# Performance work log

Measured on AMD Instinct MI355X. Metric: run time of the kernel, lower is better.

The kernel has to match this reference:

```python
import jax, jax.numpy as jnp
import numpy as np

B, S, H, NH = 4, 1024, 1024, 16
HD = H // NH
CAUSAL_HEADS = 4
META_HEADS = NH // 4
CAUSAL_W = 0.7                      # cognitive_state['reasoning']['causal_active'] > 0.5 -> branch on
META_W = ((0.9 - 0.8) / 0.2) * 0.3  # awareness_level = 0.9 > 0.8 -> meta branch on, blend = 0.15


def _mha(xq, xkv, Win, bi, Wout, bout, nh):
    """torch nn.MultiheadAttention (batch_first) with packed in_proj [H, 3H]."""
    b, sq, h = xq.shape
    sk = xkv.shape[1]
    hd = h // nh
    q = (xq @ Win[:, :h] + bi[:h]).reshape(b, sq, nh, hd).transpose(0, 2, 1, 3)
    k = (xkv @ Win[:, h:2 * h] + bi[h:2 * h]).reshape(b, sk, nh, hd).transpose(0, 2, 1, 3)
    v = (xkv @ Win[:, 2 * h:] + bi[2 * h:]).reshape(b, sk, nh, hd).transpose(0, 2, 1, 3)
    scores = jnp.einsum('bhqd,bhkd->bhqk', q, k) / jnp.sqrt(jnp.asarray(hd, q.dtype))
    probs = jax.nn.softmax(scores, axis=-1)
    ctx = jnp.einsum('bhqk,bhkd->bhqd', probs, v)
    return ctx.transpose(0, 2, 1, 3).reshape(b, sq, h) @ Wout + bout


def _forward(hidden_states, cons_vec, Wq, bq, Wk, bk, Wv, bv, cg_W, cg_b, am_W, am_b,
             ca_Win, ca_bin, ca_Wout, ca_bout, mc_Win, mc_bin, mc_Wout, mc_bout, Wo, bo):
    b, s, h = hidden_states.shape
    q = (hidden_states @ Wq + bq).reshape(b, s, NH, HD).transpose(0, 2, 1, 3)
    k = (hidden_states @ Wk + bk).reshape(b, s, NH, HD).transpose(0, 2, 1, 3)
    v = (hidden_states @ Wv + bv).reshape(b, s, NH, HD).transpose(0, 2, 1, 3)
    scores = jnp.einsum('bhqd,bhkd->bhqk', q, k) / jnp.sqrt(jnp.asarray(HD, q.dtype))
    # consciousness-gated score modulation: sigmoid(gate(x) + awareness(cons_vec)) per (query, head)
    mod = jax.nn.sigmoid(hidden_states @ cg_W + cg_b + (cons_vec @ am_W + am_b))  # [B,S,NH]
    scores = scores * mod.transpose(0, 2, 1)[..., None]  # [B,NH,S,1] broadcast over keys
    probs = jax.nn.softmax(scores, axis=-1)
    ctx = jnp.einsum('bhqk,bhkd->bhqd', probs, v).transpose(0, 2, 1, 3).reshape(b, s, h)
    # causal MHA branch (active: causal_active=0.7 > 0.5)
    causal_ctx = _mha(hidden_states, hidden_states, ca_Win, ca_bin, ca_Wout, ca_bout, CAUSAL_HEADS)
    ctx = ctx * (1.0 - CAUSAL_W) + causal_ctx * CAUSAL_W
    # metacognitive MHA branch (active: awareness=0.9 > 0.8)
    meta_ctx = _mha(ctx, ctx, mc_Win, mc_bin, mc_Wout, mc_bout, META_HEADS)
    ctx = ctx * (1.0 - META_W) + meta_ctx * META_W
    return ctx @ Wo + bo


def setup_inputs() -> dict:
    key = jax.random.key(0)
    ks = jax.random.split(key, 16)
    sc = 0.02
    d = {
        'hidden_states': jax.random.normal(ks[0], (B, S, H), jnp.float32),
        'cons_vec': jax.random.uniform(ks[1], (16,), jnp.float32),
        'Wq': jax.random.normal(ks[2], (H, H), jnp.float32) * sc, 'bq': jnp.zeros((H,), jnp.float32),
        'Wk': jax.random.normal(ks[3], (H, H), jnp.float32) * sc, 'bk': jnp.zeros((H,), jnp.float32),
        'Wv': jax.random.normal(ks[4], (H, H), jnp.float32) * sc, 'bv': jnp.zeros((H,), jnp.float32),
        'cg_W': jax.random.normal(ks[5], (H, NH), jnp.float32) * sc, 'cg_b': jnp.zeros((NH,), jnp.float32),
        'am_W': jax.random.normal(ks[6], (16, NH), jnp.float32) * sc, 'am_b': jnp.zeros((NH,), jnp.float32),
        'ca_Win': jax.random.normal(ks[7], (H, 3 * H), jnp.float32) * sc, 'ca_bin': jnp.zeros((3 * H,), jnp.float32),
        'ca_Wout': jax.random.normal(ks[8], (H, H), jnp.float32) * sc, 'ca_bout': jnp.zeros((H,), jnp.float32),
        'mc_Win': jax.random.normal(ks[9], (H, 3 * H), jnp.float32) * sc, 'mc_bin': jnp.zeros((3 * H,), jnp.float32),
        'mc_Wout': jax.random.normal(ks[10], (H, H), jnp.float32) * sc, 'mc_bout': jnp.zeros((H,), jnp.float32),
        'Wo': jax.random.normal(ks[11], (H, H), jnp.float32) * sc, 'bo': jnp.zeros((H,), jnp.float32),
    }
    return d


def reference(hidden_states, cons_vec, Wq, bq, Wk, bk, Wv, bv, cg_W, cg_b, am_W, am_b,
              ca_Win, ca_bin, ca_Wout, ca_bout, mc_Win, mc_bin, mc_Wout, mc_bout, Wo, bo):
    return _forward(hidden_states, cons_vec, Wq, bq, Wk, bk, Wv, bv, cg_W, cg_b, am_W, am_b,
                    ca_Win, ca_bin, ca_Wout, ca_bout, mc_Win, mc_bin, mc_Wout, mc_bout, Wo, bo)
```

## Files before the change

### kernel.cpp

```cpp
#include <hip/hip_runtime.h>
#include <stdint.h>

typedef unsigned short u16;
typedef __attribute__((ext_vector_type(8))) short short8;
typedef __attribute__((ext_vector_type(4))) float f32x4;
typedef __attribute__((ext_vector_type(16))) float f32x16;

#define MFMA16(a,b,c) __builtin_amdgcn_mfma_f32_16x16x32_bf16((a),(b),(c),0,0,0)
#define MFMA32(a,b,c) __builtin_amdgcn_mfma_f32_32x32x16_bf16((a),(b),(c),0,0,0)

__device__ __forceinline__ float fast_exp2(float x) {
  return __builtin_amdgcn_exp2f(x);
}

__device__ __forceinline__ u16 f2bf(float f) {
  union { float f; uint32_t u; } v; v.f = f;
  uint32_t r = v.u + 0x7FFFu + ((v.u >> 16) & 1u);
  return (u16)(r >> 16);
}
__device__ __forceinline__ float bf2f(uint32_t u) {
  union { uint32_t i; float f; } v; v.i = u << 16; return v.f;
}
__device__ __forceinline__ void async_copy16(void* lds, const void* g) {
  __builtin_amdgcn_global_load_lds(
      (const __attribute__((address_space(1))) uint32_t*)g,
      (__attribute__((address_space(3))) uint32_t*)lds, 16, 0, 0);
}

__device__ __forceinline__ void transpose8x8(uint32_t r[4], int lane8) {
  uint32_t a0, a1, a2, a3;
  a0 = __shfl_xor(r[0], 4); a1 = __shfl_xor(r[1], 4);
  a2 = __shfl_xor(r[2], 4); a3 = __shfl_xor(r[3], 4);
  if (lane8 & 4) { r[0] = a2; r[1] = a3; } else { r[2] = a0; r[3] = a1; }
  a0 = __shfl_xor(r[0], 2); a1 = __shfl_xor(r[1], 2);
  a2 = __shfl_xor(r[2], 2); a3 = __shfl_xor(r[3], 2);
  if (lane8 & 2) { r[0] = a1; r[2] = a3; } else { r[1] = a0; r[3] = a2; }
  a0 = __shfl_xor(r[0], 1); a1 = __shfl_xor(r[1], 1);
  a2 = __shfl_xor(r[2], 1); a3 = __shfl_xor(r[3], 1);
  uint32_t sel = (lane8 & 1) ? 0x03020706u : 0x05040100u;
  r[0] = __builtin_amdgcn_perm(a0, r[0], sel);
  r[1] = __builtin_amdgcn_perm(a1, r[1], sel);
  r[2] = __builtin_amdgcn_perm(a2, r[2], sel);
  r[3] = __builtin_amdgcn_perm(a3, r[3], sel);
}

__global__ __launch_bounds__(256) void castmod_kernel(
    const float* __restrict__ X, u16* __restrict__ Xbf,
    const float* __restrict__ cgW, const float* __restrict__ cgb,
    const float* __restrict__ cons, const float* __restrict__ amW,
    const float* __restrict__ amb, float* __restrict__ modp) {
  __shared__ float xs[1024];
  __shared__ float part[16][16];
  __shared__ float am[16];
  int row = blockIdx.x, t = threadIdx.x;
  {
    float4 v = ((const float4*)(X + (size_t)row * 1024))[t];
    xs[t * 4 + 0] = v.x; xs[t * 4 + 1] = v.y; xs[t * 4 + 2] = v.z; xs[t * 4 + 3] = v.w;
    uint2 o;
    o.x = (uint32_t)f2bf(v.x) | ((uint32_t)f2bf(v.y) << 16);
    o.y = (uint32_t)f2bf(v.z) | ((uint32_t)f2bf(v.w) << 16);
    ((uint2*)Xbf)[(size_t)row * 256 + t] = o;
  }
  if (t < 16) {
    float a = amb[t];
#pragma unroll
    for (int i = 0; i < 16; i++) a += cons[i] * amW[i * 16 + t];
    am[t] = a;
  }
  __syncthreads();
  int h = t & 15, ch = t >> 4;
  float p = 0.f;
#pragma unroll 8
  for (int k = ch * 64; k < ch * 64 + 64; k++) p += xs[k] * cgW[k * 16 + h];
  part[ch][h] = p;
  __syncthreads();
  if (t < 16) {
    float s = cgb[t] + am[t];
#pragma unroll
    for (int c = 0; c < 16; c++) s += part[c][t];
    int b = row >> 10, si = row & 1023;
    modp[((size_t)(b * 16 + t)) * 1024 + si] = 0.18033688f / (1.f + __expf(-s));
  }
}

struct PrepArgs {
  const float* src[12];
  u16* dst[12];
  int sstride[12];
  const float* cabin; const float* bq; const float* bk; const float* bv;
  float* biasBig; float* lbuf;
};
__global__ __launch_bounds__(256) void prep_weights(PrepArgs p) {
  int z = blockIdx.z;
  int tx = threadIdx.x & 31, ty = threadIdx.x >> 5;
  if (z < 12) {
    __shared__ float tile[32][33];
    const float* __restrict__ in = p.src[z];
    u16* __restrict__ out = p.dst[z];
    int sstr = p.sstride[z];
    int c0 = blockIdx.x * 32, r0 = blockIdx.y * 32;
#pragma unroll
    for (int j = 0; j < 4; j++)
      tile[ty + j * 8][tx] = in[(size_t)(r0 + ty + j * 8) * sstr + c0 + tx];
    __syncthreads();
#pragma unroll
    for (int j = 0; j < 4; j++)
      out[(size_t)(c0 + ty + j * 8) * 1024 + r0 + tx] = f2bf(tile[tx][ty + j * 8]);
  } else {
    int id = blockIdx.y * 32 + blockIdx.x, t = threadIdx.x;
    if (id < 24) {
      int i = id * 256 + t;
      float v;
      if (i < 3072) v = p.cabin[i];
      else if (i < 4096) v = p.bq[i - 3072];
      else if (i < 5120) v = p.bk[i - 4096];
      else v = p.bv[i - 5120];
      p.biasBig[i] = v;
    } else if (id < 152) {
      p.lbuf[(id - 24) * 256 + t] = 0.f;
    }
  }
}

template <int OUT_F32, int HAS_EXTRA, int BN>
__global__ __launch_bounds__(256, 3) void gemm_bt(
    const u16* __restrict__ A, const u16* __restrict__ Bt,
    const float* __restrict__ bias, const u16* __restrict__ extra,
    float alpha, float beta, void* __restrict__ Cout, int M, int N, int K) {
  constexpr int NJ = BN / 32;
  __shared__ u16 As[128 * 64];
  __shared__ u16 Bs[BN * 64];
  const int t = threadIdx.x;
  const int w = t >> 6, l = t & 63, lm = l & 15, lg = l >> 4;
  const int wm = w & 1, wn = w >> 1;
  const int m0 = blockIdx.y * 128, n0 = blockIdx.x * BN;
  const int rl = l >> 3, gsrc8 = ((l & 7) ^ (rl & 7)) * 8;
  const f32x4 fzero = {0.f, 0.f, 0.f, 0.f};
  f32x4 acc[4][NJ];
#pragma unroll
  for (int i = 0; i < 4; i++)
#pragma unroll
    for (int j = 0; j < NJ; j++) acc[i][j] = fzero;

  for (int kt = 0; kt < K; kt += 64) {
    __syncthreads();
#pragma unroll
    for (int c = 0; c < 4; c++) {
      int rb = c * 32 + w * 8;
      async_copy16(&As[rb * 64], A + (size_t)(m0 + rb + rl) * K + kt + gsrc8);
    }
#pragma unroll
    for (int c = 0; c < BN / 32; c++) {
      int rb = c * 32 + w * 8;
      async_copy16(&Bs[rb * 64], Bt + (size_t)(n0 + rb + rl) * K + kt + gsrc8);
    }
    __syncthreads();
#pragma unroll
    for (int kk = 0; kk < 2; kk++) {
      short8 af[4], bf[NJ];
      const int gph = ((kk * 4 + lg) ^ (lm & 7)) * 8;
#pragma unroll
      for (int i = 0; i < 4; i++)
        af[i] = *(const short8*)&As[(wm * 64 + i * 16 + lm) * 64 + gph];
#pragma unroll
      for (int j = 0; j < NJ; j++)
        bf[j] = *(const short8*)&Bs[(wn * (BN / 2) + j * 16 + lm) * 64 + gph];
#pragma unroll
      for (int i = 0; i < 4; i++)
#pragma unroll
        for (int j = 0; j < NJ; j++) acc[i][j] = MFMA16(af[i], bf[j], acc[i][j]);
    }
  }
#pragma unroll
  for (int i = 0; i < 4; i++) {
    int row0 = m0 + wm * 64 + i * 16 + lg * 4;
#pragma unroll
    for (int j = 0; j < NJ; j++) {
      int col = n0 + wn * (BN / 2) + j * 16 + lm;
      float bc = bias[col];
#pragma unroll
      for (int r = 0; r < 4; r++) {
        size_t idx = (size_t)(row0 + r) * N + col;
        float v = acc[i][j][r] + bc;
        if constexpr (HAS_EXTRA) v = alpha * v + beta * bf2f(extra[idx]);
        if constexpr (OUT_F32) ((float*)Cout)[idx] = v;
        else ((u16*)Cout)[idx] = f2bf(v);
      }
    }
  }
}

__global__ __launch_bounds__(256, 3) void gemm_in3(
    const u16* __restrict__ A, const u16* __restrict__ BtBig,
    const float* __restrict__ bias, u16* __restrict__ qkOut,
    u16* __restrict__ Vtb, u16* __restrict__ qkvm) {
  constexpr int K = 1024;
  __shared__ u16 As[128 * 64];
  __shared__ u16 Bs[128 * 64];
  const int t = threadIdx.x;
  const int w = t >> 6, l = t & 63, lm = l & 15, lg = l >> 4;
  const int wm = w & 1, wn = w >> 1;
  const int m0 = blockIdx.y * 128, n0 = blockIdx.x * 128;
  const int rl = l >> 3, gsrc8 = ((l & 7) ^ (rl & 7)) * 8;
  const f32x4 fzero = {0.f, 0.f, 0.f, 0.f};
  f32x4 acc[4][4];
#pragma unroll
  for (int i = 0; i < 4; i++)
#pragma unroll
    for (int j = 0; j < 4; j++) acc[i][j] = fzero;

  for (int kt = 0; kt < K; kt += 64) {
    __syncthreads();
#pragma unroll
    for (int c = 0; c < 4; c++) {
      int rb = c * 32 + w * 8;
      async_copy16(&As[rb * 64], A + (size_t)(m0 + rb + rl) * K + kt + gsrc8);
      async_copy16(&Bs[rb * 64], BtBig + (size_t)(n0 + rb + rl) * K + kt + gsrc8);
    }
    __syncthreads();
#pragma unroll
    for (int kk = 0; kk < 2; kk++) {
      short8 af[4], bf[4];
      const int gph = ((kk * 4 + lg) ^ (lm & 7)) * 8;
#pragma unroll
      for (int i = 0; i < 4; i++)
        af[i] = *(const short8*)&As[(wm * 64 + i * 16 + lm) * 64 + gph];
#pragma unroll
      for (int j = 0; j < 4; j++)
        bf[j] = *(const short8*)&Bs[(wn * 64 + j * 16 + lm) * 64 + gph];
#pragma unroll
      for (int i = 0; i < 4; i++)
#pragma unroll
        for (int j = 0; j < 4; j++) acc[i][j] = MFMA16(af[i], bf[j], acc[i][j]);
    }
  }
#pragma unroll
  for (int i = 0; i < 4; i++) {
    int row0 = m0 + wm * 64 + i * 16 + lg * 4;
#pragma unroll
    for (int j = 0; j < 4; j++) {
      int col = n0 + wn * 64 + j * 16 + lm;
      float bc = bias[col];
      if (col < 2048) {
#pragma unroll
        for (int r = 0; r < 4; r++)
          qkOut[(size_t)(row0 + r) * 2048 + col] = f2bf(acc[i][j][r] + bc);
      } else if (col < 3072) {
        int b = row0 >> 10, q0 = row0 & 1023;
        int z = b * 4 + ((col - 2048) >> 8), d = (col - 2048) & 255;
        union { u16 pk[4]; uint2 v; } u;
#pragma unroll
        for (int r = 0; r < 4; r++) u.pk[r] = f2bf(acc[i][j][r] + bc);
        *(uint2*)&Vtb[((size_t)z * 256 + d) * 1024 + q0] = u.v;
      } else {
#pragma unroll
        for (int r = 0; r < 4; r++)
          qkvm[(size_t)(row0 + r) * 3072 + col - 3072] = f2bf(acc[i][j][r] + bc);
      }
    }
  }
}

__device__ __forceinline__ void qk_body(
    char* smem, const u16* __restrict__ qk, u16* __restrict__ P,
    float* __restrict__ lrow, float scale2, int nb, int mb, int z) {
  constexpr int QKS = 2048;
  u16* As = (u16*)smem;
  u16* Bs = (u16*)(smem + 128 * 64 * 2);
  const int t = threadIdx.x;
  const int w = t >> 6, l = t & 63, lm = l & 15, lg = l >> 4;
  const int wm = w & 1, wn = w >> 1;
  const int b = z >> 2, h = z & 3;
  const int m0 = mb * 128, n0 = nb * 128;
  const u16* Abase = qk + ((size_t)b << 10) * QKS + h * 256;
  const u16* Bbase = qk + ((size_t)b << 10) * QKS + 1024 + h * 256;
  const int rl = l >> 3, gsrc8 = ((l & 7) ^ (rl & 7)) * 8;
  const f32x4 fzero = {0.f, 0.f, 0.f, 0.f};
  f32x4 acc[4][4];
#pragma unroll
  for (int i = 0; i < 4; i++)
#pragma unroll
    for (int j = 0; j < 4; j++) acc[i][j] = fzero;

#pragma unroll
  for (int kt = 0; kt < 256; kt += 64) {
    __syncthreads();
#pragma unroll
    for (int c = 0; c < 4; c++) {
      int rb = c * 32 + w * 8;
      async_copy16(&As[rb * 64], Abase + (size_t)(m0 + rb + rl) * QKS + kt + gsrc8);
      async_copy16(&Bs[rb * 64], Bbase + (size_t)(n0 + rb + rl) * QKS + kt + gsrc8);
    }
    __syncthreads();
#pragma unroll
    for (int kk = 0; kk < 2; kk++) {
      short8 af[4], bf[4];
      const int gph = ((kk * 4 + lg) ^ (lm & 7)) * 8;
#pragma unroll
      for (int i = 0; i < 4; i++)
        af[i] = *(const short8*)&As[(wm * 64 + i * 16 + lm) * 64 + gph];
#pragma unroll
      for (int j = 0; j < 4; j++)
        bf[j] = *(const short8*)&Bs[(wn * 64 + j * 16 + lm) * 64 + gph];
#pragma unroll
      for (int i = 0; i < 4; i++)
#pragma unroll
        for (int j = 0; j < 4; j++) acc[i][j] = MFMA16(af[i], bf[j], acc[i][j]);
    }
  }
  u16* Pz = P + ((size_t)z << 20);
#pragma unroll
  for (int i = 0; i < 4; i++) {
    int row0 = m0 + wm * 64 + i * 16 + lg * 4;
    float rsum[4] = {0.f, 0.f, 0.f, 0.f};
#pragma unroll
    for (int j = 0; j < 4; j++) {
      int col = n0 + wn * 64 + j * 16 + lm;
#pragma unroll
      for (int r = 0; r < 4; r++) {
        float p = fast_exp2(acc[i][j][r] * scale2);
        rsum[r] += p;
        Pz[(size_t)(row0 + r) * 1024 + col] = f2bf(p);
      }
    }
#pragma unroll
    for (int r = 0; r < 4; r++) {
      float s = rsum[r];
#pragma unroll
      for (int sh = 1; sh <= 8; sh <<= 1) s += __shfl_xor(s, sh);
      if (lm == 0) atomicAdd(&lrow[(z << 10) + row0 + r], s);
    }
  }
}

__global__ __launch_bounds__(256, 3) void gemm_qk_exp(
    const u16* __restrict__ qk, u16* __restrict__ P, float* __restrict__ lrow,
    float scale2) {
  __shared__ char smem[2 * 128 * 64 * 2];
  qk_body(smem, qk, P, lrow, scale2, blockIdx.x, blockIdx.y, blockIdx.z);
}

__device__ __forceinline__ void flash_body(
    char* smem, const u16* __restrict__ qkv, const float* __restrict__ modp,
    u16* __restrict__ outp, int fid) {
  constexpr int S = 1024, W3 = 3072, HD = 64, BKV = 128;
  constexpr int VSTR = 136, PSTR = 136;
  u16* Ks = (u16*)smem;
  u16* Vt = (u16*)(smem + 16384);
  u16* Ps = (u16*)(smem + 16384 + 17408);

  const int t = threadIdx.x, w = t >> 6, l = t & 63, l31 = l & 31, hl = l >> 5;
  const int rest = fid >> 3;
  const int q0 = (rest & 7) * 128;
  const int bh = (fid & 7) + 8 * (rest >> 3);
  const int b = bh >> 4, h = bh & 15;
  const size_t rowbase = (size_t)b * S;
  const int qw = q0 + w * 32;

  const int oc = t >> 3, kvo = t & 7;
  const int sd0 = (oc & 7) * 8;
  const int skvg = (oc >> 3) * 8;

  short8 qf[4];
  {
    const u16* qp = qkv + (rowbase + qw + l31) * W3 + h * HD + hl * 8;
#pragma unroll
    for (int ks = 0; ks < 4; ks++) qf[ks] = *(const short8*)(qp + ks * 16);
  }
  float rs[16], lsum[16];
#pragma unroll
  for (int reg = 0; reg < 16; reg++) {
    int qloc = (reg & 3) + 8 * (reg >> 2) + 4 * hl;
    rs[reg] = modp[(size_t)bh * S + qw + qloc];
    lsum[reg] = 0.f;
  }
  f32x16 oacc[2];
#pragma unroll
  for (int d = 0; d < 2; d++)
#pragma unroll
    for (int i = 0; i < 16; i++) oacc[d][i] = 0.f;

  for (int kb = 0; kb < S; kb += BKV) {
    __syncthreads();
#pragma unroll
    for (int c = 0; c < 4; c++) {
      int rb = c * 32 + w * 8;
      int row = rb + (l >> 3);
      int gsrc = ((l & 7) ^ (row & 7)) * 8;
      async_copy16(&Ks[rb * HD],
                   qkv + (rowbase + kb + row) * W3 + 1024 + h * HD + gsrc);
    }
#pragma unroll
    for (int c = 0; c < 4; c++) {
      int kv = c * 32 + skvg + kvo;
      union { short8 s; uint32_t u[4]; } vv, vo;
      vv.s = *(const short8*)(qkv + (rowbase + kb + kv) * W3 + 2048 + h * HD + sd0);
      uint32_t r[4] = {vv.u[0], vv.u[1], vv.u[2], vv.u[3]};
      transpose8x8(r, kvo);
      vo.u[0] = r[0]; vo.u[1] = r[1]; vo.u[2] = r[2]; vo.u[3] = r[3];
      *(short8*)&Vt[(sd0 + kvo) * VSTR + c * 32 + skvg] = vo.s;
    }
    __syncthreads();

    f32x16 sacc[4];
#pragma unroll
    for (int n = 0; n < 4; n++)
#pragma unroll
      for (int i = 0; i < 16; i++) sacc[n][i] = 0.f;
#pragma unroll
    for (int n = 0; n < 4; n++) {
      int krow = n * 32 + l31;
#pragma unroll
      for (int ks = 0; ks < 4; ks++) {
        int g = ks * 2 + hl;
        short8 kf = *(const short8*)&Ks[krow * HD + ((g ^ (krow & 7)) * 8)];
        sacc[n] = MFMA32(qf[ks], kf, sacc[n]);
      }
    }
#pragma unroll
    for (int n = 0; n < 4; n++) {
#pragma unroll
      for (int reg = 0; reg < 16; reg++) {
        float p = fast_exp2(sacc[n][reg] * rs[reg]);
        lsum[reg] += p;
        int qloc = (reg & 3) + 8 * (reg >> 2) + 4 * hl;
        Ps[(w * 32 + qloc) * PSTR + n * 32 + l31] = f2bf(p);
      }
    }
#pragma unroll
    for (int ks = 0; ks < 8; ks++) {
      short8 pa = *(const short8*)&Ps[(w * 32 + l31) * PSTR + ks * 16 + hl * 8];
#pragma unroll
      for (int d = 0; d < 2; d++) {
        short8 vb = *(const short8*)&Vt[(d * 32 + l31) * VSTR + ks * 16 + hl * 8];
        oacc[d] = MFMA32(pa, vb, oacc[d]);
      }
    }
  }
  float invl[16];
#pragma unroll
  for (int reg = 0; reg < 16; reg++) {
    float s = lsum[reg];
#pragma unroll
    for (int sh = 1; sh <= 16; sh <<= 1) s += __shfl_xor(s, sh);
    invl[reg] = 1.f / s;
  }
#pragma unroll
  for (int d = 0; d < 2; d++) {
#pragma unroll
    for (int reg = 0; reg < 16; reg++) {
      int qloc = (reg & 3) + 8 * (reg >> 2) + 4 * hl;
      outp[(rowbase + qw + qloc) * 1024 + h * HD + d * 32 + l31] =
          f2bf(oacc[d][reg] * invl[reg]);
    }
  }
}

__global__ __launch_bounds__(256, 2) void fused_qk_flash(
    const u16* __restrict__ qkvm, const float* __restrict__ modp,
    u16* __restrict__ ctxm, const u16* __restrict__ caQK,
    u16* __restrict__ P, float* __restrict__ lrow, float scale2) {
  __shared__ char smem[16384 + 17408 + 34816];
  const int bid = blockIdx.x;
  const int q3 = bid / 3, m3 = bid - q3 * 3;
  if (m3 == 2) {
    flash_body(smem, qkvm, modp, ctxm, q3);
  } else {
    int qid = q3 * 2 + m3;
    qk_body(smem, caQK, P, lrow, scale2, qid & 7, (qid >> 3) & 7, qid >> 6);
  }
}

__global__ __launch_bounds__(256, 3) void gemm_pv(
    const u16* __restrict__ P, const u16* __restrict__ Vtb,
    const float* __restrict__ lrow, u16* __restrict__ outp) {
  constexpr int K = 1024, BN = 64, NJ = 2;
  __shared__ u16 As[128 * 64];
  __shared__ u16 Bs[BN * 64];
  const int t = threadIdx.x;
  const int w = t >> 6, l = t & 63, lm = l & 15, lg = l >> 4;
  const int wm = w & 1, wn = w >> 1;
  const int z = blockIdx.z, b = z >> 2, h = z & 3;
  const int m0 = blockIdx.y * 128, n0 = blockIdx.x * BN;
  const u16* Abase = P + ((size_t)z << 20);
  const u16* Bbase = Vtb + ((size_t)z << 18);
  const int rl = l >> 3, gsrc8 = ((l & 7) ^ (rl & 7)) * 8;
  const f32x4 fzero = {0.f, 0.f, 0.f, 0.f};
  f32x4 acc[4][NJ];
#pragma unroll
  for (int i = 0; i < 4; i++)
#pragma unroll
    for (int j = 0; j < NJ; j++) acc[i][j] = fzero;

  for (int kt = 0; kt < K; kt += 64) {
    __syncthreads();
#pragma unroll
    for (int c = 0; c < 4; c++) {
      int rb = c * 32 + w * 8;
      async_copy16(&As[rb * 64], Abase + (size_t)(m0 + rb + rl) * K + kt + gsrc8);
    }
#pragma unroll
    for (int c = 0; c < BN / 32; c++) {
      int rb = c * 32 + w * 8;
      async_copy16(&Bs[rb * 64], Bbase + (size_t)(n0 + rb + rl) * K + kt + gsrc8);
    }
    __syncthreads();
#pragma unroll
    for (int kk = 0; kk < 2; kk++) {
      short8 af[4], bf[NJ];
      const int gph = ((kk * 4 + lg) ^ (lm & 7)) * 8;
#pragma unroll
      for (int i = 0; i < 4; i++)
        af[i] = *(const short8*)&As[(wm * 64 + i * 16 + lm) * 64 + gph];
#pragma unroll
      for (int j = 0; j < NJ; j++)
        bf[j] = *(const short8*)&Bs[(wn * (BN / 2) + j * 16 + lm) * 64 + gph];
#pragma unroll
      for (int i = 0; i < 4; i++)
#pragma unroll
        for (int j = 0; j < NJ; j++) acc[i][j] = MFMA16(af[i], bf[j], acc[i][j]);
    }
  }
#pragma unroll
  for (int i = 0; i < 4; i++) {
    int row0 = m0 + wm * 64 + i * 16 + lg * 4;
    float invl[4];
#pragma unroll
    for (int r = 0; r < 4; r++) invl[r] = 1.f / lrow[(z << 10) + row0 + r];
#pragma unroll
    for (int j = 0; j < NJ; j++) {
      int col = n0 + wn * (BN / 2) + j * 16 + lm;
#pragma unroll
      for (int r = 0; r < 4; r++)
        outp[(size_t)((b << 10) + row0 + r) * 1024 + h * 256 + col] =
            f2bf(acc[i][j][r] * invl[r]);
    }
  }
}

extern "C" void kernel_launch(void* const* d_in, const int* in_sizes, int n_in,
                              void* d_out, int out_size, void* d_ws, size_t ws_size,
                              hipStream_t stream) {
  (void)in_sizes; (void)n_in; (void)out_size; (void)ws_size;
  const float* X      = (const float*)d_in[0];
  const float* cons   = (const float*)d_in[1];
  const float* Wq     = (const float*)d_in[2];  const float* bq     = (const float*)d_in[3];
  const float* Wk     = (const float*)d_in[4];  const float* bk     = (const float*)d_in[5];
  const float* Wv     = (const float*)d_in[6];  const float* bv     = (const float*)d_in[7];
  const float* cgW    = (const float*)d_in[8];  const float* cgb    = (const float*)d_in[9];
  const float* amW    = (const float*)d_in[10]; const float* amb    = (const float*)d_in[11];
  const float* caWin  = (const float*)d_in[12]; const float* cabin  = (const float*)d_in[13];
  const float* caWout = (const float*)d_in[14]; const float* cabout = (const float*)d_in[15];
  const float* mcWin  = (const float*)d_in[16]; const float* mcbin  = (const float*)d_in[17];
  const float* mcWout = (const float*)d_in[18]; const float* mcbout = (const float*)d_in[19];
  const float* Wo     = (const float*)d_in[20]; const float* bo     = (const float*)d_in[21];

  char* ws = (char*)d_ws;
  size_t off = 0;
  auto alloc = [&](size_t bytes) -> void* {
    void* p = ws + off; off += (bytes + 255) & ~(size_t)255; return p;
  };
  u16*    Xbf     = (u16*)alloc((size_t)4096 * 1024 * 2);
  u16*    BtBig   = (u16*)alloc((size_t)6144 * 1024 * 2);
  u16*    mcWinT  = (u16*)alloc((size_t)3072 * 1024 * 2);
  u16*    caWoutT = (u16*)alloc((size_t)1024 * 1024 * 2);
  u16*    mcWoutT = (u16*)alloc((size_t)1024 * 1024 * 2);
  u16*    WoT     = (u16*)alloc((size_t)1024 * 1024 * 2);
  float*  biasBig = (float*)alloc(6144 * 4);
  float*  modb    = (float*)alloc((size_t)64 * 1024 * 4);
  u16*    caQK    = (u16*)alloc((size_t)4096 * 2048 * 2);
  u16*    qkvm    = (u16*)alloc((size_t)4096 * 3072 * 2);
  u16*    actx    = (u16*)alloc((size_t)4096 * 1024 * 2);
  u16*    ctxm    = (u16*)alloc((size_t)4096 * 1024 * 2);
  u16*    ctx1    = (u16*)alloc((size_t)4096 * 1024 * 2);
  u16*    Pbuf    = (u16*)alloc((size_t)16 * 1024 * 1024 * 2);
  u16*    Vtb     = (u16*)alloc((size_t)16 * 256 * 1024 * 2);
  float*  lbuf    = (float*)alloc((size_t)2 * 16384 * 4);
  float*  l_ca    = lbuf;
  float*  l_mc    = lbuf + 16384;
  u16*    mcQK    = caQK;
  u16*    mctx    = ctxm;
  u16*    ctx2    = actx;

  const float SC2 = 1.4426950408889634f / 16.f;

  castmod_kernel<<<4096, 256, 0, stream>>>(X, Xbf, cgW, cgb, cons, amW, amb, modb);
  {
    PrepArgs pa;
    for (int s = 0; s < 3; s++) {
      pa.src[s] = caWin + s * 1024; pa.dst[s] = BtBig + (size_t)s * 1024 * 1024;
      pa.sstride[s] = 3072;
    }
    pa.src[3] = Wq; pa.dst[3] = BtBig + (size_t)3072 * 1024; pa.sstride[3] = 1024;
    pa.src[4] = Wk; pa.dst[4] = BtBig + (size_t)4096 * 1024; pa.sstride[4] = 1024;
    pa.src[5] = Wv; pa.dst[5] = BtBig + (size_t)5120 * 1024; pa.sstride[5] = 1024;
    for (int s = 0; s < 3; s++) {
      pa.src[6 + s] = mcWin + s * 1024; pa.dst[6 + s] = mcWinT + (size_t)s * 1024 * 1024;
      pa.sstride[6 + s] = 3072;
    }
    pa.src[9]  = caWout; pa.dst[9]  = caWoutT; pa.sstride[9]  = 1024;
    pa.src[10] = mcWout; pa.dst[10] = mcWoutT; pa.sstride[10] = 1024;
    pa.src[11] = Wo;     pa.dst[11] = WoT;     pa.sstride[11] = 1024;
    pa.cabin = cabin; pa.bq = bq; pa.bk = bk; pa.bv = bv;
    pa.biasBig = biasBig; pa.lbuf = lbuf;
    prep_weights<<<dim3(32, 32, 13), 256, 0, stream>>>(pa);
  }

  gemm_in3<<<dim3(48, 32), 256, 0, stream>>>(Xbf, BtBig, biasBig, caQK, Vtb, qkvm);
  fused_qk_flash<<<1536, 256, 0, stream>>>(qkvm, modb, ctxm, caQK, Pbuf, l_ca, SC2);
  gemm_pv<<<dim3(4, 8, 16), 256, 0, stream>>>(Pbuf, Vtb, l_ca, actx);
  gemm_bt<0, 1, 64><<<dim3(16, 32), 256, 0, stream>>>(actx, caWoutT, cabout, ctxm, 0.7f, 0.3f,
                                                      ctx1, 4096, 1024, 1024);
  gemm_in3<<<dim3(24, 32), 256, 0, stream>>>(ctx1, mcWinT, mcbin, mcQK, Vtb, qkvm );
  gemm_qk_exp<<<dim3(8, 8, 16), 256, 0, stream>>>(mcQK, Pbuf, l_mc, SC2);
  gemm_pv<<<dim3(4, 8, 16), 256, 0, stream>>>(Pbuf, Vtb, l_mc, mctx);
  gemm_bt<0, 1, 64><<<dim3(16, 32), 256, 0, stream>>>(mctx, mcWoutT, mcbout, ctx1, 0.15f, 0.85f,
                                                      ctx2, 4096, 1024, 1024);
  gemm_bt<1, 0, 64><<<dim3(16, 32), 256, 0, stream>>>(ctx2, WoT, bo, nullptr, 0.f, 0.f,
                                                      d_out, 4096, 1024, 1024);
}
```

Baseline: 446.7 us.

## Keep flash attention probabilities in registers via transposed MFMA layout

Computes S^T by swapping the MFMA operands so each lane holds one query row. The exponentiated probabilities can then be packed to bf16 and exchanged across half-waves with shuffles, feeding the PV MFMA directly instead of going through an LDS round trip. The per-row modulation scale and row sum collapse to a single scalar per lane, and the output stores become vectorized. The smaller LDS footprint allows launch bounds to rise to 4 blocks per CU, at the risk of register pressure and of the qk_body branch sharing this kernel needing more LDS.

```diff
diff --git a/kernel.cpp b/kernel.cpp
--- a/kernel.cpp
+++ b/kernel.cpp
@@ -20,6 +20,9 @@
 }
 __device__ __forceinline__ float bf2f(uint32_t u) {
   union { uint32_t i; float f; } v; v.i = u << 16; return v.f;
+}
+__device__ __forceinline__ uint32_t pack_bf16_rne(float lo, float hi) {
+  return (uint32_t)f2bf(lo) | ((uint32_t)f2bf(hi) << 16);
 }
 __device__ __forceinline__ void async_copy16(void* lds, const void* g) {
   __builtin_amdgcn_global_load_lds(
@@ -344,10 +347,9 @@
     char* smem, const u16* __restrict__ qkv, const float* __restrict__ modp,
     u16* __restrict__ outp, int fid) {
   constexpr int S = 1024, W3 = 3072, HD = 64, BKV = 128;
-  constexpr int VSTR = 136, PSTR = 136;
+  constexpr int VSTR = 136;
   u16* Ks = (u16*)smem;
   u16* Vt = (u16*)(smem + 16384);
-  u16* Ps = (u16*)(smem + 16384 + 17408);
 
   const int t = threadIdx.x, w = t >> 6, l = t & 63, l31 = l & 31, hl = l >> 5;
   const int rest = fid >> 3;
@@ -367,13 +369,8 @@
 #pragma unroll
     for (int ks = 0; ks < 4; ks++) qf[ks] = *(const short8*)(qp + ks * 16);
   }
-  float rs[16], lsum[16];
-#pragma unroll
-  for (int reg = 0; reg < 16; reg++) {
-    int qloc = (reg & 3) + 8 * (reg >> 2) + 4 * hl;
-    rs[reg] = modp[(size_t)bh * S + qw + qloc];
-    lsum[reg] = 0.f;
-  }
+  const float rs = modp[(size_t)bh * S + qw + l31];
+  float lsum = 0.f;
   f32x16 oacc[2];
 #pragma unroll
   for (int d = 0; d < 2; d++)
@@ -402,65 +399,70 @@
     }
     __syncthreads();
 
-    f32x16 sacc[4];
-#pragma unroll
-    for (int n = 0; n < 4; n++)
-#pragma unroll
-      for (int i = 0; i < 16; i++) sacc[n][i] = 0.f;
 #pragma unroll
     for (int n = 0; n < 4; n++) {
-      int krow = n * 32 + l31;
+      f32x16 st;
+#pragma unroll
+      for (int i = 0; i < 16; i++) st[i] = 0.f;
+      const int krow = n * 32 + l31;
 #pragma unroll
       for (int ks = 0; ks < 4; ks++) {
         int g = ks * 2 + hl;
         short8 kf = *(const short8*)&Ks[krow * HD + ((g ^ (krow & 7)) * 8)];
-        sacc[n] = MFMA32(qf[ks], kf, sacc[n]);
+        st = MFMA32(kf, qf[ks], st);
       }
-    }
-#pragma unroll
-    for (int n = 0; n < 4; n++) {
-#pragma unroll
-      for (int reg = 0; reg < 16; reg++) {
-        float p = fast_exp2(sacc[n][reg] * rs[reg]);
-        lsum[reg] += p;
-        int qloc = (reg & 3) + 8 * (reg >> 2) + 4 * hl;
-        Ps[(w * 32 + qloc) * PSTR + n * 32 + l31] = f2bf(p);
+      uint32_t pk8[8];
+#pragma unroll
+      for (int tt = 0; tt < 4; tt++) {
+#pragma unroll
+        for (int s = 0; s < 2; s++) {
+          float p0 = fast_exp2(st[tt * 4 + 2 * s] * rs);
+          float p1 = fast_exp2(st[tt * 4 + 2 * s + 1] * rs);
+          lsum += p0 + p1;
+          pk8[tt * 2 + s] = pack_bf16_rne(p0, p1);
+        }
       }
-    }
-#pragma unroll
-    for (int ks = 0; ks < 8; ks++) {
-      short8 pa = *(const short8*)&Ps[(w * 32 + l31) * PSTR + ks * 16 + hl * 8];
-#pragma unroll
-      for (int d = 0; d < 2; d++) {
-        short8 vb = *(const short8*)&Vt[(d * 32 + l31) * VSTR + ks * 16 + hl * 8];
-        oacc[d] = MFMA32(pa, vb, oacc[d]);
+#pragma unroll
+      for (int k2 = 0; k2 < 2; k2++) {
+        const int ta = 2 * k2, tb = ta + 1;
+        uint32_t pw[4];
+#pragma unroll
+        for (int s = 0; s < 2; s++) {
+          uint32_t A = pk8[ta * 2 + s], B = pk8[tb * 2 + s];
+          uint32_t Ax = __shfl_xor(A, 32), Bx = __shfl_xor(B, 32);
+          pw[s] = hl ? Bx : A;
+          pw[2 + s] = hl ? B : Ax;
+        }
+        union { uint32_t u[4]; short8 s8; } pt;
+        pt.u[0] = pw[0]; pt.u[1] = pw[1]; pt.u[2] = pw[2]; pt.u[3] = pw[3];
+        const int ks = 2 * n + k2;
+#pragma unroll
+        for (int dt = 0; dt < 2; dt++) {
+          short8 vb = *(const short8*)&Vt[(dt * 32 + l31) * VSTR + ks * 16 + hl * 8];
+          oacc[dt] = MFMA32(vb, pt.s8, oacc[dt]);
+        }
       }
     }
   }
-  float invl[16];
-#pragma unroll
-  for (int reg = 0; reg < 16; reg++) {
-    float s = lsum[reg];
-#pragma unroll
-    for (int sh = 1; sh <= 16; sh <<= 1) s += __shfl_xor(s, sh);
-    invl[reg] = 1.f / s;
-  }
-#pragma unroll
-  for (int d = 0; d < 2; d++) {
-#pragma unroll
-    for (int reg = 0; reg < 16; reg++) {
-      int qloc = (reg & 3) + 8 * (reg >> 2) + 4 * hl;
-      outp[(rowbase + qw + qloc) * 1024 + h * HD + d * 32 + l31] =
-          f2bf(oacc[d][reg] * invl[reg]);
-    }
-  }
-}
-
-__global__ __launch_bounds__(256, 2) void fused_qk_flash(
+  float sfull = lsum + __shfl_xor(lsum, 32);
+  const float invl = 1.f / sfull;
+#pragma unroll
+  for (int dt = 0; dt < 2; dt++) {
+#pragma unroll
+    for (int tt = 0; tt < 4; tt++) {
+      union { u16 pkv[4]; uint2 v; } u;
+#pragma unroll
+      for (int r = 0; r < 4; r++) u.pkv[r] = f2bf(oacc[dt][tt * 4 + r] * invl);
+      *(uint2*)&outp[(rowbase + qw + l31) * 1024 + h * HD + dt * 32 + tt * 8 + hl * 4] = u.v;
+    }
+  }
+}
+
+__global__ __launch_bounds__(256, 4) void fused_qk_flash(
     const u16* __restrict__ qkvm, const float* __restrict__ modp,
     u16* __restrict__ ctxm, const u16* __restrict__ caQK,
     u16* __restrict__ P, float* __restrict__ lrow, float scale2) {
-  __shared__ char smem[16384 + 17408 + 34816];
+  __shared__ char smem[33792];
   const int bid = blockIdx.x;
   const int q3 = bid / 3, m3 = bid - q3 * 3;
   if (m3 == 2) {
```

After: 431.6 us. -3.4%, faster.
